# Kernel optimization log

Hardware: AMD Instinct MI355X
Metric: run time of the kernel (lower is better)

The kernel has to match this reference:

```python
import jax, jax.numpy as jnp
import numpy as np

B, L_P, L_E = 4, 768, 256
D_P, D_E = 2048, 1024
H, HKV, HD = 8, 1, 256
MAX_WAVELENGTH = 10000.0


def _rope(x, positions):
    """Apply RoPE to x [B, L, h, D] with positions [B, L] (Gemma half-split style)."""
    dtype = x.dtype
    x = x.astype(jnp.float32)
    d = x.shape[-1]
    d_half = d // 2
    inv_freq = 1.0 / (MAX_WAVELENGTH ** (2.0 / d * jnp.arange(d_half, dtype=jnp.float32)))
    freqs = positions.astype(jnp.float32)[..., None] * inv_freq  # (B, L, d_half)
    cos = jnp.cos(freqs)[:, :, None, :]  # (B, L, 1, d_half)
    sin = jnp.sin(freqs)[:, :, None, :]
    x1, x2 = jnp.split(x, 2, axis=-1)
    out = jnp.concatenate([x1 * cos - x2 * sin, x2 * cos + x1 * sin], axis=-1)
    return out.astype(dtype)


def setup_inputs() -> dict:
    key = jax.random.key(0)
    ks = jax.random.split(key, 12)
    s = 0.02
    inp = {
        "pali_embeds": jax.random.normal(ks[0], (B, L_P, D_P), jnp.float32),
        "expert_embeds": jax.random.normal(ks[1], (B, L_E, D_E), jnp.float32),
        "position_ids": jnp.sort(jax.random.randint(ks[2], (B, L_P + L_E), 0, 8192), axis=-1),
        "attention_mask": jax.random.normal(ks[3], (B, L_P + L_E, L_P + L_E), jnp.float32),
        "use_cache": 0,
        # weights stored (in_dim, out_dim), no bias per defaults
        "wq_p": jax.random.normal(ks[4], (D_P, H * HD), jnp.float32) * s,
        "wk_p": jax.random.normal(ks[5], (D_P, HKV * HD), jnp.float32) * s,
        "wv_p": jax.random.normal(ks[6], (D_P, HKV * HD), jnp.float32) * s,
        "wo_p": jax.random.normal(ks[7], (H * HD, D_P), jnp.float32) * s,
        "wq_e": jax.random.normal(ks[8], (D_E, H * HD), jnp.float32) * s,
        "wk_e": jax.random.normal(ks[9], (D_E, HKV * HD), jnp.float32) * s,
        "wv_e": jax.random.normal(ks[10], (D_E, HKV * HD), jnp.float32) * s,
        "wo_e": jax.random.normal(ks[11], (H * HD, D_E), jnp.float32) * s,
    }
    return inp


def reference(pali_embeds, expert_embeds, position_ids, attention_mask, use_cache,
              wq_p, wk_p, wv_p, wo_p, wq_e, wk_e, wv_e, wo_e):
    # use_cache == 0: prefill path without KV cache (cache fill/append is identity math here)
    Bq = pali_embeds.shape[0]
    # per-stream QKV projections, reshape to (B, L, h, D)
    q = jnp.concatenate([
        (pali_embeds @ wq_p).reshape(Bq, L_P, H, HD),
        (expert_embeds @ wq_e).reshape(Bq, L_E, H, HD)], axis=1)
    k = jnp.concatenate([
        (pali_embeds @ wk_p).reshape(Bq, L_P, HKV, HD),
        (expert_embeds @ wk_e).reshape(Bq, L_E, HKV, HD)], axis=1)
    v = jnp.concatenate([
        (pali_embeds @ wv_p).reshape(Bq, L_P, HKV, HD),
        (expert_embeds @ wv_e).reshape(Bq, L_E, HKV, HD)], axis=1)
    q = _rope(q, position_ids)
    k = _rope(k, position_ids)
    # GQA with 1 KV head: broadcast over query heads (== repeat_interleave)
    scale = 1.0 / jnp.sqrt(jnp.float32(HD))
    # scores: (B, H, Lq, Lk); k has single kv head -> squeeze and broadcast
    scores = jnp.einsum('bqhd,bkd->bhqk', q, k[:, :, 0, :]) * scale
    scores = scores + attention_mask[:, None, :, :]
    attn = jax.nn.softmax(scores, axis=-1)
    out = jnp.einsum('bhqk,bkd->bqhd', attn, v[:, :, 0, :])  # (B, L, H, D)
    out = out.reshape(Bq, L_P + L_E, H * HD)
    out_p = out[:, :L_P] @ wo_p
    out_e = out[:, L_P:] @ wo_e
    return out_p, out_e
```

## Files before the change

kernel.cpp:

```cpp
#include <hip/hip_runtime.h>
#include <hip/hip_bf16.h>
#include <math.h>

#define L_TOT 1024
#define HD 256
#define LDQKV 2560

typedef __bf16 bf16x8 __attribute__((ext_vector_type(8)));
typedef __bf16 bf16x4 __attribute__((ext_vector_type(4)));
typedef float f32x4 __attribute__((ext_vector_type(4)));

__device__ __forceinline__ void gld_lds16(const __bf16* g, __bf16* l) {
  __builtin_amdgcn_global_load_lds(
      (const __attribute__((address_space(1))) void*)g,
      (__attribute__((address_space(3))) void*)l, 16, 0, 0);
}

__device__ __forceinline__ void do_cvt(const float* __restrict__ in, __bf16* __restrict__ out,
                                       int i) {
  float4 v = ((const float4*)in)[i];
  bf16x4 o;
  o[0] = (__bf16)v.x; o[1] = (__bf16)v.y; o[2] = (__bf16)v.z; o[3] = (__bf16)v.w;
  ((bf16x4*)out)[i] = o;
}

__device__ __forceinline__ void do_transpose(const float* __restrict__ W, __bf16* __restrict__ Wt,
                                             int K, int N, int rem, int tid, float (*t)[33]) {
  const int tiles_x = N >> 5;
  const int n0 = (rem % tiles_x) * 32, k0 = (rem / tiles_x) * 32;
  const int tx = tid & 31, ty = tid >> 5;
#pragma unroll
  for (int r = 0; r < 32; r += 8)
    t[ty + r][tx] = W[(size_t)(k0 + ty + r) * N + n0 + tx];
  __syncthreads();
#pragma unroll
  for (int r = 0; r < 32; r += 8)
    Wt[(size_t)(n0 + ty + r) * K + k0 + tx] = (__bf16)t[tx][ty + r];
}

__global__ __launch_bounds__(256) void prep_kernel(
    const float* __restrict__ pali, const float* __restrict__ expe,
    const float* __restrict__ wq_p, const float* __restrict__ wk_p, const float* __restrict__ wv_p,
    const float* __restrict__ wq_e, const float* __restrict__ wk_e, const float* __restrict__ wv_e,
    const float* __restrict__ wo_p, const float* __restrict__ wo_e,
    __bf16* __restrict__ palib, __bf16* __restrict__ expeb,
    __bf16* __restrict__ WqkvpT, __bf16* __restrict__ WqkveT,
    __bf16* __restrict__ WopT, __bf16* __restrict__ WoeT)
{
  __shared__ float t[32][33];
  const int bid = blockIdx.x, tid = threadIdx.x;
  if      (bid <  6144) do_cvt(pali, palib, bid * 256 + tid);
  else if (bid <  7168) do_cvt(expe, expeb, (bid - 6144) * 256 + tid);
  else if (bid < 11264) do_transpose(wq_p, WqkvpT,                       2048, 2048, bid - 7168,  tid, t);
  else if (bid < 11776) do_transpose(wk_p, WqkvpT + (size_t)2048 * 2048, 2048,  256, bid - 11264, tid, t);
  else if (bid < 12288) do_transpose(wv_p, WqkvpT + (size_t)2304 * 2048, 2048,  256, bid - 11776, tid, t);
  else if (bid < 14336) do_transpose(wq_e, WqkveT,                       1024, 2048, bid - 12288, tid, t);
  else if (bid < 14592) do_transpose(wk_e, WqkveT + (size_t)2048 * 1024, 1024,  256, bid - 14336, tid, t);
  else if (bid < 14848) do_transpose(wv_e, WqkveT + (size_t)2304 * 1024, 1024,  256, bid - 14592, tid, t);
  else if (bid < 18944) do_transpose(wo_p, WopT,                         2048, 2048, bid - 14848, tid, t);
  else                  do_transpose(wo_e, WoeT,                         2048, 1024, bid - 18944, tid, t);
}

template <typename OutT>
__device__ __forceinline__ void gemm_body(
    const __bf16* __restrict__ A, const __bf16* __restrict__ Wt, OutT* __restrict__ C,
    int La, int K, int A_Ls, int A_off, int C_Ls, int C_off, int ldc,
    int m0, int n0, __bf16* As, __bf16* Bs, int tid)
{
  const int wave = tid >> 6, lane = tid & 63;
  const int lrow = lane >> 2;
  const int k8   = lane & 3;

  const __bf16 *ag0, *ag1;
  {
    int m_a0 = m0 + wave * 16 + lrow;
    int m_a1 = m_a0 + 64;
    int b0 = m_a0 / La, b1 = m_a1 / La;
    ag0 = A + (size_t)(b0 * A_Ls + A_off + m_a0 - b0 * La) * K + k8 * 8;
    ag1 = A + (size_t)(b1 * A_Ls + A_off + m_a1 - b1 * La) * K + k8 * 8;
  }
  const __bf16* bg0 = Wt + (size_t)(n0 + wave * 16 + lrow) * K + k8 * 8;
  const __bf16* bg1 = bg0 + (size_t)64 * K;
  __bf16* al0 = As + wave * 512;
  __bf16* al1 = As + (4 + wave) * 512;
  __bf16* bl0 = Bs + wave * 512;
  __bf16* bl1 = Bs + (4 + wave) * 512;

  const int wm = (wave & 1) * 64, wn = (wave >> 1) * 64;
  const int fr = lane & 15, quad = lane >> 4;

  f32x4 acc[4][4];
#pragma unroll
  for (int i = 0; i < 4; ++i)
#pragma unroll
    for (int j = 0; j < 4; ++j) acc[i][j] = (f32x4){0.f, 0.f, 0.f, 0.f};

  for (int kk = 0; kk < K; kk += 32) {
    gld_lds16(ag0 + kk, al0);
    gld_lds16(ag1 + kk, al1);
    gld_lds16(bg0 + kk, bl0);
    gld_lds16(bg1 + kk, bl1);
    __syncthreads();
    bf16x8 af[4], bfr[4];
#pragma unroll
    for (int mt = 0; mt < 4; ++mt)
      af[mt] = *(const bf16x8*)(As + (wm + mt * 16 + fr) * 32 + quad * 8);
#pragma unroll
    for (int nt = 0; nt < 4; ++nt)
      bfr[nt] = *(const bf16x8*)(Bs + (wn + nt * 16 + fr) * 32 + quad * 8);
#pragma unroll
    for (int mt = 0; mt < 4; ++mt)
#pragma unroll
      for (int nt = 0; nt < 4; ++nt)
        acc[mt][nt] = __builtin_amdgcn_mfma_f32_16x16x32_bf16(af[mt], bfr[nt], acc[mt][nt], 0, 0, 0);
    __syncthreads();
  }

#pragma unroll
  for (int mt = 0; mt < 4; ++mt) {
#pragma unroll
    for (int r = 0; r < 4; ++r) {
      int m = m0 + wm + mt * 16 + quad * 4 + r;
      int b = m / La;
      OutT* crow = C + (size_t)(b * C_Ls + C_off + m - b * La) * ldc + n0 + wn + fr;
#pragma unroll
      for (int nt = 0; nt < 4; ++nt) crow[nt * 16] = (OutT)acc[mt][nt][r];
    }
  }
}

__global__ __launch_bounds__(256) void gemm_qkv_kernel(
    const __bf16* __restrict__ palib, const __bf16* __restrict__ expeb,
    const __bf16* __restrict__ WqkvpT, const __bf16* __restrict__ WqkveT,
    __bf16* __restrict__ QKV)
{
  __shared__ __bf16 As[128 * 32];
  __shared__ __bf16 Bs[128 * 32];
  const int idx = blockIdx.x, tid = threadIdx.x;
  if (idx < 480) {
    gemm_body<__bf16>(palib, WqkvpT, QKV, 768, 2048, 768, 0, L_TOT, 0, LDQKV,
                      (idx / 20) * 128, (idx % 20) * 128, As, Bs, tid);
  } else {
    int j = idx - 480;
    gemm_body<__bf16>(expeb, WqkveT, QKV, 256, 1024, 256, 0, L_TOT, 768, LDQKV,
                      (j / 20) * 128, (j % 20) * 128, As, Bs, tid);
  }
}

__global__ __launch_bounds__(256) void gemm_out_kernel(
    const __bf16* __restrict__ Ab, const __bf16* __restrict__ WopT,
    const __bf16* __restrict__ WoeT, float* __restrict__ out)
{
  __shared__ __bf16 As[128 * 32];
  __shared__ __bf16 Bs[128 * 32];
  const int idx = blockIdx.x, tid = threadIdx.x;
  if (idx < 384) {
    gemm_body<float>(Ab, WopT, out, 768, 2048, 1024, 0, 768, 0, 2048,
                     (idx / 16) * 128, (idx % 16) * 128, As, Bs, tid);
  } else {
    int j = idx - 384;
    gemm_body<float>(Ab, WoeT, out + (size_t)4 * 768 * 2048, 256, 2048, 1024, 768, 256, 0, 1024,
                     (j / 8) * 128, (j % 8) * 128, As, Bs, tid);
  }
}

__global__ __launch_bounds__(256) void rope_kernel(
    __bf16* __restrict__ x, const int* __restrict__ pos)
{
  int idx = blockIdx.x * 256 + threadIdx.x;
  int j = idx & 127;
  int t = idx >> 7;
  int hh = t % 9;
  int bl = t / 9;
  int b = bl >> 10;
  int l = bl & (L_TOT - 1);
  int col = (hh < 8) ? hh * HD : 2048;
  float p = (float)pos[b * L_TOT + l];
  float f = p * expf(-(float)j * (9.210340371976184f / 128.f));
  float s, c;
  sincosf(f, &s, &c);
  size_t base = (size_t)bl * LDQKV + col;
  float x1 = (float)x[base + j], x2 = (float)x[base + 128 + j];
  x[base + j]       = (__bf16)(x1 * c - x2 * s);
  x[base + 128 + j] = (__bf16)(x2 * c + x1 * s);
}

__global__ __launch_bounds__(256) void transpose_v_kernel(
    const __bf16* __restrict__ QKV, __bf16* __restrict__ Vt)
{
  __shared__ __bf16 t[32][33];
  const int b = blockIdx.z, d0 = blockIdx.x * 32, l0 = blockIdx.y * 32;
  const int tx = threadIdx.x & 31, ty = threadIdx.x >> 5;
#pragma unroll
  for (int r = 0; r < 32; r += 8)
    t[ty + r][tx] = QKV[(size_t)(b * L_TOT + l0 + ty + r) * LDQKV + 2304 + d0 + tx];
  __syncthreads();
#pragma unroll
  for (int r = 0; r < 32; r += 8)
    Vt[(size_t)(b * HD + d0 + ty + r) * L_TOT + l0 + tx] = t[tx][ty + r];
}

__global__ __launch_bounds__(256) void attn_mfma_kernel(
    const __bf16* __restrict__ QKV, const __bf16* __restrict__ Vt,
    const float* __restrict__ mask, __bf16* __restrict__ O)
{
  const int tid  = threadIdx.x;
  const int wave = tid >> 6, lane = tid & 63;
  const int m    = lane & 15, quad = lane >> 4;
  const int h = blockIdx.y, b = blockIdx.z;
  const int q0 = blockIdx.x * 64 + wave * 16;

  __shared__ __align__(16) __bf16 Ks[2][32 * 256];
  __shared__ __align__(16) __bf16 Vs[2][256 * 32];
  __shared__ __align__(16) __bf16 Ps[4][16][40];

  bf16x8 qf[8];
  {
    const __bf16* qrow = QKV + (size_t)(b * L_TOT + q0 + m) * LDQKV + h * HD + quad * 8;
#pragma unroll
    for (int f = 0; f < 8; ++f) qf[f] = *(const bf16x8*)(qrow + f * 32);
  }

  const int krow_l = lane >> 5;
  const int vd_l   = lane >> 2;
  const int vg_l   = lane & 3;

  size_t ksrc[4], vsrc[4];
#pragma unroll
  for (int i = 0; i < 4; ++i) {
    int c = wave * 4 + i;
    int r = 2 * c + krow_l;
    int colg = ((lane & 31) - r) & 31;
    ksrc[i] = (size_t)(b * L_TOT + r) * LDQKV + 2048 + colg * 8;
    int d = c * 16 + vd_l;
    int gg = (vg_l - ((d >> 1) & 3)) & 3;
    vsrc[i] = ((size_t)(b * HD + d)) * L_TOT + gg * 8;
  }

  const float* mk = mask + (size_t)b * L_TOT * L_TOT + (size_t)(q0 + quad * 4) * L_TOT + m;

  f32x4 Oacc[16];
#pragma unroll
  for (int i = 0; i < 16; ++i) Oacc[i] = (f32x4){0.f, 0.f, 0.f, 0.f};
  float mrow[4] = {-1e30f, -1e30f, -1e30f, -1e30f};
  float lrow[4] = {0.f, 0.f, 0.f, 0.f};

#pragma unroll
  for (int i = 0; i < 4; ++i) {
    int c = wave * 4 + i;
    gld_lds16(QKV + ksrc[i], &Ks[0][c * 512]);
    gld_lds16(Vt + vsrc[i], &Vs[0][c * 512]);
  }
  float mcur[2][4];
#pragma unroll
  for (int nb = 0; nb < 2; ++nb)
#pragma unroll
    for (int r = 0; r < 4; ++r) mcur[nb][r] = mk[(size_t)r * L_TOT + nb * 16];

  for (int it = 0; it < 32; ++it) {
    const int kt = it * 32;
    const int buf = it & 1;
    __syncthreads();

    if (it + 1 < 32) {
#pragma unroll
      for (int i = 0; i < 4; ++i) {
        int c = wave * 4 + i;
        gld_lds16(QKV + ksrc[i] + (size_t)(kt + 32) * LDQKV, &Ks[buf ^ 1][c * 512]);
        gld_lds16(Vt + vsrc[i] + (kt + 32), &Vs[buf ^ 1][c * 512]);
      }
    }
    float mnext[2][4];
    if (it + 1 < 32) {
#pragma unroll
      for (int nb = 0; nb < 2; ++nb)
#pragma unroll
        for (int r = 0; r < 4; ++r)
          mnext[nb][r] = mk[(size_t)r * L_TOT + (kt + 32) + nb * 16];
    }

    f32x4 S[2];
#pragma unroll
    for (int nb = 0; nb < 2; ++nb) {
      int row = nb * 16 + m;
      f32x4 se = (f32x4){0.f, 0.f, 0.f, 0.f};
      f32x4 so = (f32x4){0.f, 0.f, 0.f, 0.f};
#pragma unroll
      for (int kf = 0; kf < 8; ++kf) {
        bf16x8 kf8 = *(const bf16x8*)(&Ks[buf][0] + row * 256 + (((kf << 2) + quad + row) & 31) * 8);
        if (kf & 1) so = __builtin_amdgcn_mfma_f32_16x16x32_bf16(qf[kf], kf8, so, 0, 0, 0);
        else        se = __builtin_amdgcn_mfma_f32_16x16x32_bf16(qf[kf], kf8, se, 0, 0, 0);
      }
      S[nb] = se + so;
    }
#pragma unroll
    for (int nb = 0; nb < 2; ++nb)
#pragma unroll
      for (int r = 0; r < 4; ++r)
        S[nb][r] = S[nb][r] * 0.0625f + mcur[nb][r];
    float mx[4];
#pragma unroll
    for (int r = 0; r < 4; ++r) mx[r] = fmaxf(S[0][r], S[1][r]);
#pragma unroll
    for (int off = 1; off < 16; off <<= 1)
#pragma unroll
      for (int r = 0; r < 4; ++r)
        mx[r] = fmaxf(mx[r], __shfl_xor(mx[r], off, 64));
    float al[4];
#pragma unroll
    for (int r = 0; r < 4; ++r) {
      float mn = fmaxf(mrow[r], mx[r]);
      al[r] = __expf(mrow[r] - mn);
      mrow[r] = mn;
    }
    float rs[4] = {0.f, 0.f, 0.f, 0.f};
#pragma unroll
    for (int nb = 0; nb < 2; ++nb)
#pragma unroll
      for (int r = 0; r < 4; ++r) {
        float p = __expf(S[nb][r] - mrow[r]);
        rs[r] += p;
        Ps[wave][quad * 4 + r][nb * 16 + m] = (__bf16)p;
      }
#pragma unroll
    for (int off = 1; off < 16; off <<= 1)
#pragma unroll
      for (int r = 0; r < 4; ++r)
        rs[r] += __shfl_xor(rs[r], off, 64);
#pragma unroll
    for (int r = 0; r < 4; ++r) lrow[r] = lrow[r] * al[r] + rs[r];
#pragma unroll
    for (int nb2 = 0; nb2 < 16; ++nb2)
#pragma unroll
      for (int r = 0; r < 4; ++r) Oacc[nb2][r] *= al[r];
    bf16x8 pf = *(const bf16x8*)&Ps[wave][m][quad * 8];
#pragma unroll
    for (int nb2 = 0; nb2 < 16; ++nb2) {
      int d = nb2 * 16 + m;
      bf16x8 vfrag = *(const bf16x8*)(&Vs[buf][0] + d * 32 + ((quad + ((d >> 1) & 3)) & 3) * 8);
      Oacc[nb2] = __builtin_amdgcn_mfma_f32_16x16x32_bf16(pf, vfrag, Oacc[nb2], 0, 0, 0);
    }
#pragma unroll
    for (int nb = 0; nb < 2; ++nb)
#pragma unroll
      for (int r = 0; r < 4; ++r) mcur[nb][r] = mnext[nb][r];
  }
  float invl[4];
#pragma unroll
  for (int r = 0; r < 4; ++r) invl[r] = 1.f / lrow[r];
  __bf16* orow = O + (size_t)(b * L_TOT + q0 + quad * 4) * 2048 + h * HD + m;
#pragma unroll
  for (int nb2 = 0; nb2 < 16; ++nb2)
#pragma unroll
    for (int r = 0; r < 4; ++r)
      orow[(size_t)r * 2048 + nb2 * 16] = (__bf16)(Oacc[nb2][r] * invl[r]);
}

extern "C" void kernel_launch(void* const* d_in, const int* in_sizes, int n_in,
                              void* d_out, int out_size, void* d_ws, size_t ws_size,
                              hipStream_t stream) {
  const float* pali = (const float*)d_in[0];
  const float* expe = (const float*)d_in[1];
  const int*   pos  = (const int*)d_in[2];
  const float* mask = (const float*)d_in[3];
  const float* wq_p = (const float*)d_in[5];
  const float* wk_p = (const float*)d_in[6];
  const float* wv_p = (const float*)d_in[7];
  const float* wo_p = (const float*)d_in[8];
  const float* wq_e = (const float*)d_in[9];
  const float* wk_e = (const float*)d_in[10];
  const float* wv_e = (const float*)d_in[11];
  const float* wo_e = (const float*)d_in[12];
  float* out = (float*)d_out;

  __bf16* QKV    = (__bf16*)d_ws;
  __bf16* Ab     = QKV + (size_t)4 * 1024 * 2560;
  __bf16* palib  = Ab + (size_t)4 * 1024 * 2048;
  __bf16* expeb  = palib + (size_t)4 * 768 * 2048;
  __bf16* Vt     = expeb + (size_t)4 * 256 * 1024;
  __bf16* WqkvpT = Vt + (size_t)4 * 256 * 1024;
  __bf16* WqkveT = WqkvpT + (size_t)2560 * 2048;
  __bf16* WopT   = WqkveT + (size_t)2560 * 1024;
  __bf16* WoeT   = WopT + (size_t)2048 * 2048;

  dim3 blk(256);
  prep_kernel<<<20992, blk, 0, stream>>>(pali, expe, wq_p, wk_p, wv_p, wq_e, wk_e, wv_e,
                                         wo_p, wo_e, palib, expeb, WqkvpT, WqkveT, WopT, WoeT);
  gemm_qkv_kernel<<<640, blk, 0, stream>>>(palib, expeb, WqkvpT, WqkveT, QKV);
  rope_kernel<<<4 * 1024 * 9 * 128 / 256, blk, 0, stream>>>(QKV, pos);
  transpose_v_kernel<<<dim3(8, 32, 4), blk, 0, stream>>>(QKV, Vt);
  attn_mfma_kernel<<<dim3(16, 8, 4), blk, 0, stream>>>(QKV, Vt, mask, Ab);
  gemm_out_kernel<<<448, blk, 0, stream>>>(Ab, WopT, WoeT, out);
}
```

Measured before the change: 397.2 us.

## Merge rope and V-transpose kernels, add lazy softmax rescale and MFMA priority

Fuses the RoPE and V-transpose launches into a single kernel with a block-index split, which removes one launch. In the attention loop it skips the running-max rescale of the accumulator unless some row's max grows by more than 8, so most tiles avoid the exp and the 64 multiplies. It raises wave priority around the MFMA blocks and moves the row-sum shuffle reduction after the PV MFMAs to overlap it. The lazy rescale lets unnormalized probabilities reach up to about e^8, which is safe in fp32 but adds some precision risk in the bf16 P values.

```diff
diff --git a/kernel.cpp b/kernel.cpp
--- a/kernel.cpp
+++ b/kernel.cpp
@@ -164,40 +164,41 @@
   }
 }
 
-__global__ __launch_bounds__(256) void rope_kernel(
-    __bf16* __restrict__ x, const int* __restrict__ pos)
-{
-  int idx = blockIdx.x * 256 + threadIdx.x;
-  int j = idx & 127;
-  int t = idx >> 7;
-  int hh = t % 9;
-  int bl = t / 9;
-  int b = bl >> 10;
-  int l = bl & (L_TOT - 1);
-  int col = (hh < 8) ? hh * HD : 2048;
-  float p = (float)pos[b * L_TOT + l];
-  float f = p * expf(-(float)j * (9.210340371976184f / 128.f));
-  float s, c;
-  sincosf(f, &s, &c);
-  size_t base = (size_t)bl * LDQKV + col;
-  float x1 = (float)x[base + j], x2 = (float)x[base + 128 + j];
-  x[base + j]       = (__bf16)(x1 * c - x2 * s);
-  x[base + 128 + j] = (__bf16)(x2 * c + x1 * s);
-}
-
-__global__ __launch_bounds__(256) void transpose_v_kernel(
-    const __bf16* __restrict__ QKV, __bf16* __restrict__ Vt)
+__global__ __launch_bounds__(256) void rope_trv_kernel(
+    __bf16* __restrict__ x, const int* __restrict__ pos, __bf16* __restrict__ Vt)
 {
   __shared__ __bf16 t[32][33];
-  const int b = blockIdx.z, d0 = blockIdx.x * 32, l0 = blockIdx.y * 32;
-  const int tx = threadIdx.x & 31, ty = threadIdx.x >> 5;
-#pragma unroll
-  for (int r = 0; r < 32; r += 8)
-    t[ty + r][tx] = QKV[(size_t)(b * L_TOT + l0 + ty + r) * LDQKV + 2304 + d0 + tx];
-  __syncthreads();
-#pragma unroll
-  for (int r = 0; r < 32; r += 8)
-    Vt[(size_t)(b * HD + d0 + ty + r) * L_TOT + l0 + tx] = t[tx][ty + r];
+  const int bid = blockIdx.x, tid = threadIdx.x;
+  if (bid < 18432) {
+    int idx = bid * 256 + tid;
+    int j = idx & 127;
+    int tt = idx >> 7;
+    int hh = tt % 9;
+    int bl = tt / 9;
+    int b = bl >> 10;
+    int l = bl & (L_TOT - 1);
+    int col = (hh < 8) ? hh * HD : 2048;
+    float p = (float)pos[b * L_TOT + l];
+    float f = p * expf(-(float)j * (9.210340371976184f / 128.f));
+    float s, c;
+    sincosf(f, &s, &c);
+    size_t base = (size_t)bl * LDQKV + col;
+    float x1 = (float)x[base + j], x2 = (float)x[base + 128 + j];
+    x[base + j]       = (__bf16)(x1 * c - x2 * s);
+    x[base + 128 + j] = (__bf16)(x2 * c + x1 * s);
+  } else {
+    const int j = bid - 18432;
+    const int b = j >> 8;
+    const int d0 = (j & 7) * 32, l0 = ((j >> 3) & 31) * 32;
+    const int tx = tid & 31, ty = tid >> 5;
+#pragma unroll
+    for (int r = 0; r < 32; r += 8)
+      t[ty + r][tx] = x[(size_t)(b * L_TOT + l0 + ty + r) * LDQKV + 2304 + d0 + tx];
+    __syncthreads();
+#pragma unroll
+    for (int r = 0; r < 32; r += 8)
+      Vt[(size_t)(b * HD + d0 + ty + r) * L_TOT + l0 + tx] = t[tx][ty + r];
+  }
 }
 
 __global__ __launch_bounds__(256) void attn_mfma_kernel(
@@ -280,6 +281,7 @@
     }
 
     f32x4 S[2];
+    __builtin_amdgcn_s_setprio(1);
 #pragma unroll
     for (int nb = 0; nb < 2; ++nb) {
       int row = nb * 16 + m;
@@ -293,11 +295,14 @@
       }
       S[nb] = se + so;
     }
+    __builtin_amdgcn_s_setprio(0);
+
 #pragma unroll
     for (int nb = 0; nb < 2; ++nb)
 #pragma unroll
       for (int r = 0; r < 4; ++r)
         S[nb][r] = S[nb][r] * 0.0625f + mcur[nb][r];
+
     float mx[4];
 #pragma unroll
     for (int r = 0; r < 4; ++r) mx[r] = fmaxf(S[0][r], S[1][r]);
@@ -306,13 +311,25 @@
 #pragma unroll
       for (int r = 0; r < 4; ++r)
         mx[r] = fmaxf(mx[r], __shfl_xor(mx[r], off, 64));
-    float al[4];
-#pragma unroll
-    for (int r = 0; r < 4; ++r) {
-      float mn = fmaxf(mrow[r], mx[r]);
-      al[r] = __expf(mrow[r] - mn);
-      mrow[r] = mn;
-    }
+
+    bool need = false;
+#pragma unroll
+    for (int r = 0; r < 4; ++r) need |= (mx[r] > mrow[r] + 8.f);
+    if (__any(need)) {
+      float al[4];
+#pragma unroll
+      for (int r = 0; r < 4; ++r) {
+        float mn = fmaxf(mrow[r], mx[r]);
+        al[r] = __expf(mrow[r] - mn);
+        mrow[r] = mn;
+        lrow[r] *= al[r];
+      }
+#pragma unroll
+      for (int nb2 = 0; nb2 < 16; ++nb2)
+#pragma unroll
+        for (int r = 0; r < 4; ++r) Oacc[nb2][r] *= al[r];
+    }
+
     float rs[4] = {0.f, 0.f, 0.f, 0.f};
 #pragma unroll
     for (int nb = 0; nb < 2; ++nb)
@@ -322,24 +339,25 @@
         rs[r] += p;
         Ps[wave][quad * 4 + r][nb * 16 + m] = (__bf16)p;
       }
-#pragma unroll
-    for (int off = 1; off < 16; off <<= 1)
-#pragma unroll
-      for (int r = 0; r < 4; ++r)
-        rs[r] += __shfl_xor(rs[r], off, 64);
-#pragma unroll
-    for (int r = 0; r < 4; ++r) lrow[r] = lrow[r] * al[r] + rs[r];
-#pragma unroll
-    for (int nb2 = 0; nb2 < 16; ++nb2)
-#pragma unroll
-      for (int r = 0; r < 4; ++r) Oacc[nb2][r] *= al[r];
+
     bf16x8 pf = *(const bf16x8*)&Ps[wave][m][quad * 8];
+    __builtin_amdgcn_s_setprio(1);
 #pragma unroll
     for (int nb2 = 0; nb2 < 16; ++nb2) {
       int d = nb2 * 16 + m;
       bf16x8 vfrag = *(const bf16x8*)(&Vs[buf][0] + d * 32 + ((quad + ((d >> 1) & 3)) & 3) * 8);
       Oacc[nb2] = __builtin_amdgcn_mfma_f32_16x16x32_bf16(pf, vfrag, Oacc[nb2], 0, 0, 0);
     }
+    __builtin_amdgcn_s_setprio(0);
+
+#pragma unroll
+    for (int off = 1; off < 16; off <<= 1)
+#pragma unroll
+      for (int r = 0; r < 4; ++r)
+        rs[r] += __shfl_xor(rs[r], off, 64);
+#pragma unroll
+    for (int r = 0; r < 4; ++r) lrow[r] += rs[r];
+
 #pragma unroll
     for (int nb = 0; nb < 2; ++nb)
 #pragma unroll
@@ -387,8 +405,7 @@
   prep_kernel<<<20992, blk, 0, stream>>>(pali, expe, wq_p, wk_p, wv_p, wq_e, wk_e, wv_e,
                                          wo_p, wo_e, palib, expeb, WqkvpT, WqkveT, WopT, WoeT);
   gemm_qkv_kernel<<<640, blk, 0, stream>>>(palib, expeb, WqkvpT, WqkveT, QKV);
-  rope_kernel<<<4 * 1024 * 9 * 128 / 256, blk, 0, stream>>>(QKV, pos);
-  transpose_v_kernel<<<dim3(8, 32, 4), blk, 0, stream>>>(QKV, Vt);
+  rope_trv_kernel<<<18432 + 1024, blk, 0, stream>>>(QKV, pos, Vt);
   attn_mfma_kernel<<<dim3(16, 8, 4), blk, 0, stream>>>(QKV, Vt, mask, Ab);
   gemm_out_kernel<<<448, blk, 0, stream>>>(Ab, WopT, WoeT, out);
 }
```

Measured after the change: 439.4 us. 10.6% more time.
